# Performance work log

Hardware: AMD Instinct MI355X
Metric: run time of the kernel (lower is better)

Reference implementation:

```python
import jax, jax.numpy as jnp
import numpy as np

B, S, HID = 2, 2048, 4096
NH, NKV, HD = 32, 8, 128
SLIDING_WINDOW = 1024
ROPE_THETA = 10000.0


def setup_inputs() -> dict:
    key = jax.random.key(0)
    ks = jax.random.split(key, 6)
    hidden_states = jax.random.normal(ks[0], (B, S, HID), dtype=jnp.float32)
    attention_mask = jnp.ones((B, S), dtype=jnp.int32)
    position_ids = jnp.broadcast_to(jnp.arange(S, dtype=jnp.int32)[None, :], (B, S))
    sc = 1.0 / np.sqrt(HID)
    q_w = jax.random.normal(ks[1], (HID, NH * HD), dtype=jnp.float32) * sc
    k_w = jax.random.normal(ks[2], (HID, NKV * HD), dtype=jnp.float32) * sc
    v_w = jax.random.normal(ks[3], (HID, NKV * HD), dtype=jnp.float32) * sc
    o_w = jax.random.normal(ks[4], (NH * HD, HID), dtype=jnp.float32) * sc
    return {"hidden_states": hidden_states, "attention_mask": attention_mask,
            "position_ids": position_ids, "q_w": q_w, "k_w": k_w, "v_w": v_w, "o_w": o_w}


def _rotate_half(x):
    return jnp.concatenate((-x[..., x.shape[-1] // 2:], x[..., : x.shape[-1] // 2]), axis=-1)


def _rope_sincos(position_ids):
    # inv_freq over even dims of head_dim; emb = concat(freqs, freqs)
    inv_freq = 1.0 / ROPE_THETA ** (jnp.arange(0, HD, 2, dtype=jnp.float32) / HD)
    freqs = position_ids.astype(jnp.float32)[..., None] * inv_freq  # [B,S,HD/2]
    emb = jnp.concatenate((freqs, freqs), axis=-1)                  # [B,S,HD]
    # broadcast over heads axis: [B,S,1,HD]
    return jnp.sin(emb)[:, :, None, :], jnp.cos(emb)[:, :, None, :]


def reference(hidden_states, attention_mask, position_ids, q_w, k_w, v_w, o_w):
    b, q_len, _ = hidden_states.shape
    n_rep = NH // NKV

    q = (hidden_states @ q_w).reshape(b, q_len, NH, HD)
    k = (hidden_states @ k_w).reshape(b, q_len, NKV, HD)
    v = (hidden_states @ v_w).reshape(b, q_len, NKV, HD)

    sin_pos, cos_pos = _rope_sincos(position_ids)
    q = q * cos_pos + _rotate_half(q) * sin_pos
    k = k * cos_pos + _rotate_half(k) * sin_pos

    # GQA: repeat kv heads (repeat_interleave along head axis)
    k = jnp.repeat(k, n_rep, axis=2)  # [B,S,NH,HD]
    v = jnp.repeat(v, n_rep, axis=2)

    # sliding-window causal mask: j <= i and j >= i - sliding_window
    i = jnp.arange(q_len)[:, None]
    j = jnp.arange(q_len)[None, :]
    band = (j <= i) & (j >= i - SLIDING_WINDOW)           # [Q,K]
    mask = band[None, None] & (attention_mask[:, None, None, :] > 0)  # [B,1,Q,K]

    bias = jnp.where(mask, 0.0, jnp.finfo(jnp.float32).min)

    scale = 1.0 / jnp.sqrt(jnp.asarray(HD, dtype=jnp.float32))
    scores = jnp.einsum('bqhd,bkhd->bhqk', q, k) * scale + bias
    attn_weights = jax.nn.softmax(scores, axis=-1)
    attn_out = jnp.einsum('bhqk,bkhd->bqhd', attn_weights, v)
    attn_out = attn_out.reshape(b, q_len, HID)
    return attn_out @ o_w
```

## Files before the change

kernel.cpp:

```cpp
#include <hip/hip_runtime.h>
#include <stdint.h>
#include <stddef.h>

typedef __bf16 bf16x8 __attribute__((ext_vector_type(8)));
typedef short short8 __attribute__((ext_vector_type(8)));
typedef float floatx4 __attribute__((ext_vector_type(4)));
typedef float f32x16 __attribute__((ext_vector_type(16)));
typedef unsigned short ushort4v __attribute__((ext_vector_type(4)));
typedef unsigned int uint2v __attribute__((ext_vector_type(2)));

__device__ __forceinline__ unsigned short f2bf(float f){
  unsigned int u = __float_as_uint(f);
  u += 0x7fffu + ((u >> 16) & 1u);
  return (unsigned short)(u >> 16);
}
__device__ __forceinline__ float bf2f(unsigned short s){
  return __uint_as_float(((unsigned int)s) << 16);
}
__device__ __forceinline__ void gl2lds16(const void* g, void* l){
  __builtin_amdgcn_global_load_lds((const __attribute__((address_space(1))) void*)g,
                                   (__attribute__((address_space(3))) void*)l, 16, 0, 0);
}

__device__ __forceinline__ void transpose_body(const float* __restrict__ in,
                                               unsigned short* __restrict__ out,
                                               int Kd, int Nd, int bx, int by, int t,
                                               unsigned short* tile){
  int n0 = bx * 64, k0 = by * 64;
#pragma unroll
  for (int it = 0; it < 2; ++it){
    int rr = (t >> 3) + it * 32;
    int cc = t & 7;
    const float* src = in + (size_t)(k0 + rr) * Nd + n0 + cc * 8;
    floatx4 a = *(const floatx4*)src;
    floatx4 b = *(const floatx4*)(src + 4);
    short8 s;
#pragma unroll
    for (int j = 0; j < 4; ++j){ s[j] = (short)f2bf(a[j]); s[j + 4] = (short)f2bf(b[j]); }
    *(short8*)&tile[rr * 80 + cc * 8] = s;
  }
  __syncthreads();
#pragma unroll
  for (int it = 0; it < 2; ++it){
    int nr = (t >> 3) + it * 32;
    int kc = t & 7;
    short8 v;
#pragma unroll
    for (int j = 0; j < 8; ++j) v[j] = (short)tile[(kc * 8 + j) * 80 + nr];
    *(short8*)(out + (size_t)(n0 + nr) * Kd + k0 + kc * 8) = v;
  }
}

__global__ __launch_bounds__(256) void transpose_cvt(const float* __restrict__ in,
                                                     unsigned short* __restrict__ out,
                                                     int Kd, int Nd){
  __shared__ __align__(16) unsigned short tile[64 * 80];
  transpose_body(in, out, Kd, Nd, blockIdx.x, blockIdx.y, threadIdx.x, tile);
}

__global__ __launch_bounds__(256) void prep_fused(const float* __restrict__ hidden,
                                                  unsigned short* __restrict__ hb,
                                                  const float* __restrict__ qw,
                                                  unsigned short* __restrict__ qtw,
                                                  const float* __restrict__ kw,
                                                  unsigned short* __restrict__ kt,
                                                  const float* __restrict__ vw,
                                                  unsigned short* __restrict__ vtw){
  __shared__ __align__(16) unsigned short tile[64 * 80];
  const int bid = blockIdx.x, t = threadIdx.x;
  if (bid < 16384){
    int i = bid * 256 + t;
    floatx4 v = *(const floatx4*)(hidden + (size_t)i * 4);
    ushort4v o;
#pragma unroll
    for (int j = 0; j < 4; ++j) o[j] = f2bf(v[j]);
    *(ushort4v*)(hb + (size_t)i * 4) = o;
  } else if (bid < 20480){
    int b2 = bid - 16384;
    transpose_body(qw, qtw, 4096, 4096, b2 & 63, b2 >> 6, t, tile);
  } else if (bid < 21504){
    int b2 = bid - 20480;
    transpose_body(kw, kt, 4096, 1024, b2 & 15, b2 >> 4, t, tile);
  } else {
    int b2 = bid - 21504;
    transpose_body(vw, vtw, 4096, 1024, b2 & 15, b2 >> 4, t, tile);
  }
}

__global__ __launch_bounds__(256, 2) void gemm_bt128(
    const unsigned short* __restrict__ A,
    const unsigned short* __restrict__ Wq,
    const unsigned short* __restrict__ Wk,
    const unsigned short* __restrict__ Wv,
    unsigned short* __restrict__ oQ,
    unsigned short* __restrict__ oK,
    unsigned short* __restrict__ oVt,
    float* __restrict__ oF, int f32out)
{
  __shared__ __align__(16) unsigned short As[128 * 64];
  __shared__ __align__(16) unsigned short Bs[128 * 64];
  const int tid = threadIdx.x;
  const int w = tid >> 6, lane = tid & 63, quad = lane >> 4, l15 = lane & 15;
  const int wm64 = (w >> 1) * 64, wn64 = (w & 1) * 64;
  const int m0 = blockIdx.y * 128;
  const int n0 = blockIdx.x * 128;

  const unsigned short* Wsrc;
  int nb, region;
  if (n0 < 4096)      { Wsrc = Wq; nb = n0;        region = 0; }
  else if (n0 < 5120) { Wsrc = Wk; nb = n0 - 4096; region = 1; }
  else                { Wsrc = Wv; nb = n0 - 5120; region = 2; }

  floatx4 acc[4][4];
#pragma unroll
  for (int i = 0; i < 4; ++i)
#pragma unroll
    for (int j = 0; j < 4; ++j) acc[i][j] = (floatx4){0.f, 0.f, 0.f, 0.f};

  const int rsub = lane >> 3, csub = lane & 7;

  for (int k0 = 0; k0 < 4096; k0 += 64){
#pragma unroll
    for (int i = 0; i < 4; ++i){
      int u = i * 4 + w;
      int r = u * 8 + rsub;
      gl2lds16(A    + ((size_t)(m0 + r) << 12) + k0 + ((csub ^ (r & 7)) << 3), (char*)As + u * 1024);
      gl2lds16(Wsrc + ((size_t)(nb + r) << 12) + k0 + ((csub ^ (r & 7)) << 3), (char*)Bs + u * 1024);
    }
    __syncthreads();
#pragma unroll
    for (int ks = 0; ks < 2; ++ks){
      bf16x8 af[4], bfr[4];
#pragma unroll
      for (int mt = 0; mt < 4; ++mt){
        int r = wm64 + mt * 16 + l15;
        int kc = ks * 4 + quad;
        af[mt] = *(const bf16x8*)&As[r * 64 + ((kc ^ (r & 7)) << 3)];
      }
#pragma unroll
      for (int nt = 0; nt < 4; ++nt){
        int r = wn64 + nt * 16 + l15;
        int kc = ks * 4 + quad;
        bfr[nt] = *(const bf16x8*)&Bs[r * 64 + ((kc ^ (r & 7)) << 3)];
      }
#pragma unroll
      for (int mt = 0; mt < 4; ++mt)
#pragma unroll
        for (int nt = 0; nt < 4; ++nt)
          acc[mt][nt] = __builtin_amdgcn_mfma_f32_16x16x32_bf16(af[mt], bfr[nt], acc[mt][nt], 0, 0, 0);
    }
    __syncthreads();
  }

  if (region == 0){
    if (f32out){
#pragma unroll
      for (int mt = 0; mt < 4; ++mt)
#pragma unroll
        for (int nt = 0; nt < 4; ++nt){
          int gn = n0 + wn64 + nt * 16 + l15;
#pragma unroll
          for (int rr = 0; rr < 4; ++rr){
            int gm = m0 + wm64 + mt * 16 + quad * 4 + rr;
            oF[((size_t)gm << 12) + gn] = acc[mt][nt][rr];
          }
        }
    } else {
#pragma unroll
      for (int mt = 0; mt < 4; ++mt)
#pragma unroll
        for (int nt = 0; nt < 4; ++nt){
          int gn = n0 + wn64 + nt * 16 + l15;
#pragma unroll
          for (int rr = 0; rr < 4; ++rr){
            int gm = m0 + wm64 + mt * 16 + quad * 4 + rr;
            oQ[((size_t)gm << 12) + gn] = f2bf(acc[mt][nt][rr]);
          }
        }
    }
  } else if (region == 1){
#pragma unroll
    for (int mt = 0; mt < 4; ++mt)
#pragma unroll
      for (int nt = 0; nt < 4; ++nt){
        int gn = n0 - 4096 + wn64 + nt * 16 + l15;
#pragma unroll
        for (int rr = 0; rr < 4; ++rr){
          int gm = m0 + wm64 + mt * 16 + quad * 4 + rr;
          oK[((size_t)gm << 10) + gn] = f2bf(acc[mt][nt][rr]);
        }
      }
  } else {
#pragma unroll
    for (int mt = 0; mt < 4; ++mt){
      int gm0 = m0 + wm64 + mt * 16 + quad * 4;
      int b = gm0 >> 11, s0 = gm0 & 2047;
#pragma unroll
      for (int nt = 0; nt < 4; ++nt){
        int dg = n0 - 5120 + wn64 + nt * 16 + l15;
        int kvh = dg >> 7, d = dg & 127;
        ushort4v pk;
#pragma unroll
        for (int rr = 0; rr < 4; ++rr) pk[rr] = f2bf(acc[mt][nt][rr]);
        *(ushort4v*)(oVt + (((size_t)(b * 8 + kvh) * 128 + d) * 2048 + s0)) = pk;
      }
    }
  }
}

__global__ __launch_bounds__(512, 2) void gemm_bt256(
    const unsigned short* __restrict__ A,
    const unsigned short* __restrict__ Wq,
    const unsigned short* __restrict__ Wk,
    const unsigned short* __restrict__ Wv,
    unsigned short* __restrict__ oQ,
    unsigned short* __restrict__ oK,
    unsigned short* __restrict__ oVt,
    float* __restrict__ oF, int f32out)
{
  __shared__ __align__(16) unsigned short As[2][256 * 64];
  __shared__ __align__(16) unsigned short Bs[2][256 * 64];
  const int tid = threadIdx.x;
  const int w = tid >> 6, lane = tid & 63, quad = lane >> 4, l15 = lane & 15;
  const int wr = w >> 2, wc = w & 3;
  const int m0 = blockIdx.y * 256;
  const int n0 = blockIdx.x * 256;

  const unsigned short* Wsrc;
  int nb, region;
  if (n0 < 4096)      { Wsrc = Wq; nb = n0;        region = 0; }
  else if (n0 < 5120) { Wsrc = Wk; nb = n0 - 4096; region = 1; }
  else                { Wsrc = Wv; nb = n0 - 5120; region = 2; }

  floatx4 acc[8][4];
#pragma unroll
  for (int i = 0; i < 8; ++i)
#pragma unroll
    for (int j = 0; j < 4; ++j) acc[i][j] = (floatx4){0.f, 0.f, 0.f, 0.f};

#define STG(SRC, ROW0, H, DST, K0)                                                     \
  { _Pragma("unroll")                                                                  \
    for (int rep_ = 0; rep_ < 2; ++rep_){                                              \
      int u_ = tid + rep_ * 512;                                                       \
      int r_ = (H) * 128 + (u_ >> 3);                                                  \
      int c_ = u_ & 7;                                                                 \
      gl2lds16((SRC) + ((size_t)((ROW0) + r_) << 12) + (K0) + ((c_ ^ (r_ & 7)) << 3),  \
               (char*)(DST) + (H) * 16384 + (size_t)u_ * 16);                          \
    } }

  STG(A,    m0, 0, &As[0][0], 0);
  STG(Wsrc, nb, 0, &Bs[0][0], 0);
  STG(Wsrc, nb, 1, &Bs[0][0], 0);
  STG(A,    m0, 1, &As[0][0], 0);
  asm volatile("s_waitcnt vmcnt(4)" ::: "memory");
  __builtin_amdgcn_s_barrier();

  for (int t = 0; t < 64; ++t){
    const int cb = t & 1, nbuf = cb ^ 1;
    const int s = (t < 63) ? (t + 1) : 63;
    const int kn = s << 6;
    const unsigned short* Ac = &As[cb][0];
    const unsigned short* Bc = &Bs[cb][0];

    bf16x8 af[4][2], bf0[2][2], bf1[2][2];

#pragma unroll
    for (int i = 0; i < 4; ++i){
      int r = (wr * 4 + i) * 16 + l15;
#pragma unroll
      for (int ks = 0; ks < 2; ++ks){
        int kc = ks * 4 + quad;
        af[i][ks] = *(const bf16x8*)&Ac[r * 64 + ((kc ^ (r & 7)) << 3)];
      }
    }
#pragma unroll
    for (int j = 0; j < 2; ++j){
      int r = (wc * 2 + j) * 16 + l15;
#pragma unroll
      for (int ks = 0; ks < 2; ++ks){
        int kc = ks * 4 + quad;
        bf0[j][ks] = *(const bf16x8*)&Bc[r * 64 + ((kc ^ (r & 7)) << 3)];
      }
    }
    STG(A, m0, 0, &As[nbuf][0], kn);
    __builtin_amdgcn_s_setprio(1);
#pragma unroll
    for (int i = 0; i < 4; ++i)
#pragma unroll
      for (int j = 0; j < 2; ++j)
#pragma unroll
        for (int ks = 0; ks < 2; ++ks)
          acc[i][j] = __builtin_amdgcn_mfma_f32_16x16x32_bf16(af[i][ks], bf0[j][ks], acc[i][j], 0, 0, 0);
    __builtin_amdgcn_s_setprio(0);
    asm volatile("s_waitcnt vmcnt(4)" ::: "memory");
    __builtin_amdgcn_s_barrier();

#pragma unroll
    for (int j = 0; j < 2; ++j){
      int r = (8 + wc * 2 + j) * 16 + l15;
#pragma unroll
      for (int ks = 0; ks < 2; ++ks){
        int kc = ks * 4 + quad;
        bf1[j][ks] = *(const bf16x8*)&Bc[r * 64 + ((kc ^ (r & 7)) << 3)];
      }
    }
    STG(Wsrc, nb, 0, &Bs[nbuf][0], kn);
    __builtin_amdgcn_s_setprio(1);
#pragma unroll
    for (int i = 0; i < 4; ++i)
#pragma unroll
      for (int j = 0; j < 2; ++j)
#pragma unroll
        for (int ks = 0; ks < 2; ++ks)
          acc[i][2 + j] = __builtin_amdgcn_mfma_f32_16x16x32_bf16(af[i][ks], bf1[j][ks], acc[i][2 + j], 0, 0, 0);
    __builtin_amdgcn_s_setprio(0);
    asm volatile("s_waitcnt vmcnt(4)" ::: "memory");
    __builtin_amdgcn_s_barrier();

#pragma unroll
    for (int i = 0; i < 4; ++i){
      int r = (8 + wr * 4 + i) * 16 + l15;
#pragma unroll
      for (int ks = 0; ks < 2; ++ks){
        int kc = ks * 4 + quad;
        af[i][ks] = *(const bf16x8*)&Ac[r * 64 + ((kc ^ (r & 7)) << 3)];
      }
    }
    STG(Wsrc, nb, 1, &Bs[nbuf][0], kn);
    __builtin_amdgcn_s_setprio(1);
#pragma unroll
    for (int i = 0; i < 4; ++i)
#pragma unroll
      for (int j = 0; j < 2; ++j)
#pragma unroll
        for (int ks = 0; ks < 2; ++ks)
          acc[4 + i][2 + j] = __builtin_amdgcn_mfma_f32_16x16x32_bf16(af[i][ks], bf1[j][ks], acc[4 + i][2 + j], 0, 0, 0);
    __builtin_amdgcn_s_setprio(0);
    __builtin_amdgcn_s_barrier();

#pragma unroll
    for (int j = 0; j < 2; ++j){
      int r = (wc * 2 + j) * 16 + l15;
#pragma unroll
      for (int ks = 0; ks < 2; ++ks){
        int kc = ks * 4 + quad;
        bf0[j][ks] = *(const bf16x8*)&Bc[r * 64 + ((kc ^ (r & 7)) << 3)];
      }
    }
    STG(A, m0, 1, &As[nbuf][0], kn);
    __builtin_amdgcn_s_setprio(1);
#pragma unroll
    for (int i = 0; i < 4; ++i)
#pragma unroll
      for (int j = 0; j < 2; ++j)
#pragma unroll
        for (int ks = 0; ks < 2; ++ks)
          acc[4 + i][j] = __builtin_amdgcn_mfma_f32_16x16x32_bf16(af[i][ks], bf0[j][ks], acc[4 + i][j], 0, 0, 0);
    __builtin_amdgcn_s_setprio(0);
    asm volatile("s_waitcnt vmcnt(4)" ::: "memory");
    __builtin_amdgcn_s_barrier();
  }
#undef STG

  if (region == 0){
    if (f32out){
#pragma unroll
      for (int mi = 0; mi < 8; ++mi){
        const int row = (mi >> 2) * 128 + wr * 64 + (mi & 3) * 16 + quad * 4;
#pragma unroll
        for (int nj = 0; nj < 4; ++nj){
          const int gn = n0 + (nj >> 1) * 128 + wc * 32 + (nj & 1) * 16 + l15;
#pragma unroll
          for (int rr = 0; rr < 4; ++rr){
            const int gm = m0 + row + rr;
            oF[((size_t)gm << 12) + gn] = acc[mi][nj][rr];
          }
        }
      }
    } else {
#pragma unroll
      for (int mi = 0; mi < 8; ++mi){
        const int row = (mi >> 2) * 128 + wr * 64 + (mi & 3) * 16 + quad * 4;
#pragma unroll
        for (int nj = 0; nj < 4; ++nj){
          const int gn = n0 + (nj >> 1) * 128 + wc * 32 + (nj & 1) * 16 + l15;
#pragma unroll
          for (int rr = 0; rr < 4; ++rr){
            const int gm = m0 + row + rr;
            oQ[((size_t)gm << 12) + gn] = f2bf(acc[mi][nj][rr]);
          }
        }
      }
    }
  } else if (region == 1){
#pragma unroll
    for (int mi = 0; mi < 8; ++mi){
      const int row = (mi >> 2) * 128 + wr * 64 + (mi & 3) * 16 + quad * 4;
#pragma unroll
      for (int nj = 0; nj < 4; ++nj){
        const int gn = n0 - 4096 + (nj >> 1) * 128 + wc * 32 + (nj & 1) * 16 + l15;
#pragma unroll
        for (int rr = 0; rr < 4; ++rr){
          const int gm = m0 + row + rr;
          oK[((size_t)gm << 10) + gn] = f2bf(acc[mi][nj][rr]);
        }
      }
    }
  } else {
#pragma unroll
    for (int mi = 0; mi < 8; ++mi){
      const int gm0 = m0 + (mi >> 2) * 128 + wr * 64 + (mi & 3) * 16 + quad * 4;
      const int b = gm0 >> 11, s0 = gm0 & 2047;
#pragma unroll
      for (int nj = 0; nj < 4; ++nj){
        const int dg = n0 - 5120 + (nj >> 1) * 128 + wc * 32 + (nj & 1) * 16 + l15;
        const int kvh = dg >> 7, d = dg & 127;
        ushort4v pk;
#pragma unroll
        for (int rr = 0; rr < 4; ++rr) pk[rr] = f2bf(acc[mi][nj][rr]);
        *(ushort4v*)(oVt + (((size_t)(b * 8 + kvh) * 128 + d) * 2048 + s0)) = pk;
      }
    }
  }
}

__global__ void rope_apply_k(unsigned short* __restrict__ Qb, unsigned short* __restrict__ Kb,
                             const int* __restrict__ pos){
  int t = blockIdx.x * 256 + threadIdx.x;
  unsigned short* base;
  int row, ch;
  bool isq = (t < 1048576);
  if (isq){ row = t >> 8; int c = t & 255; base = Qb + ((size_t)row << 12) + (c >> 3) * 128; ch = c & 7; }
  else { int t2 = t - 1048576; row = t2 >> 6; int c = t2 & 63; base = Kb + ((size_t)row << 10) + (c >> 3) * 128; ch = c & 7; }
  float p = (float)pos[row];
  const float qs = 0.08838834764831845f * 1.44269504088896340736f;
  float sc_out = isq ? qs : 1.0f;
  int d0 = ch * 8;
  short8 x0 = *(short8*)(base + d0);
  short8 x1 = *(short8*)(base + d0 + 64);
  short8 y0, y1;
#pragma unroll
  for (int j = 0; j < 8; ++j){
    float ang = p * exp2f(-(float)(d0 + j) * 0.20762050593045952f);
    float sn = sinf(ang), cs = cosf(ang);
    float a  = bf2f((unsigned short)x0[j]);
    float bb = bf2f((unsigned short)x1[j]);
    y0[j] = (short)f2bf((a * cs - bb * sn) * sc_out);
    y1[j] = (short)f2bf((bb * cs + a * sn) * sc_out);
  }
  *(short8*)(base + d0)      = y0;
  *(short8*)(base + d0 + 64) = y1;
}

__global__ __launch_bounds__(256, 2) void flash_swa(
    const unsigned short* __restrict__ Q,
    const unsigned short* __restrict__ K,
    const unsigned short* __restrict__ Vt,
    const int* __restrict__ amask,
    unsigned short* __restrict__ attn)
{
  __shared__ __align__(16) unsigned short Kl[2][64 * 128];
  __shared__ __align__(16) unsigned short Vl[2][128 * 64];
  __shared__ __align__(16) unsigned int   Pl[4][1024];
  const int h = blockIdx.y, b = blockIdx.z;
  const int kv = h >> 2;
  const int tid = threadIdx.x, w = tid >> 6, lane = tid & 63;
  const int l31 = lane & 31, hi = lane >> 5, hi4 = hi << 2;
  const int qb = blockIdx.x * 128;
  const int t0 = qb >> 6;
  const int qw0 = qb + w * 32;
  const int aw = t0 + (w >> 1);

  bool anybad = false;
  {
    const int* ap = amask + b * 2048 + lane * 32;
#pragma unroll
    for (int i = 0; i < 8; ++i){
      int4 mv = *(const int4*)(ap + i * 4);
      anybad |= (mv.x <= 0) | (mv.y <= 0) | (mv.z <= 0) | (mv.w <= 0);
    }
  }
  const bool allv = (__ballot(anybad) == 0ull);

  bf16x8 qf[8];
  {
    const unsigned short* qbase = Q + (((size_t)(b * 2048 + qw0 + l31)) << 12) + h * 128;
#pragma unroll
    for (int ds = 0; ds < 8; ++ds) qf[ds] = *(const bf16x8*)(qbase + ds * 16 + hi * 8);
  }

  f32x16 acco[4];
#pragma unroll
  for (int i = 0; i < 4; ++i)
#pragma unroll
    for (int j = 0; j < 16; ++j) acco[i][j] = 0.f;
  float m_i = -1e30f, l_i = 0.f;

  const int jb0 = (t0 >= 16) ? (t0 - 16) : 0;
  const int jtend = t0 + 1;

#define STAGE_KV(JT, BUF)                                                                  \
  {                                                                                        \
    const int k0s = (JT) * 64;                                                             \
    _Pragma("unroll")                                                                      \
    for (int i_ = 0; i_ < 4; ++i_){                                                        \
      int u_ = i_ * 4 + w;                                                                 \
      int r_ = u_ * 4 + (lane >> 4);                                                       \
      int c_ = lane & 15;                                                                  \
      gl2lds16(K + (((size_t)(b * 2048 + k0s + r_)) << 10) + kv * 128 + ((c_ ^ (r_ & 15)) << 3), \
               (char*)Kl[BUF] + u_ * 1024);                                                \
    }                                                                                      \
    _Pragma("unroll")                                                                      \
    for (int i_ = 0; i_ < 4; ++i_){                                                        \
      int u_ = i_ * 4 + w;                                                                 \
      int d_ = u_ * 8 + (lane >> 3);                                                       \
      int c_ = lane & 7;                                                                   \
      gl2lds16(Vt + ((size_t)(b * 8 + kv) * 128 + d_) * 2048 + k0s + ((c_ ^ (d_ & 7)) << 3), \
               (char*)Vl[BUF] + u_ * 1024);                                                \
    }                                                                                      \
  }

  STAGE_KV(jb0, 0);
  __syncthreads();

  unsigned int* Pw = &Pl[w][0];
  int cur = 0;
  for (int jt = jb0; jt <= jtend; ++jt){
    if (jt < jtend) STAGE_KV(jt + 1, cur ^ 1);

    const bool active = (jt >= aw - 16) && (jt <= aw);
    if (active){
      const int k0 = jt * 64;
      const unsigned short* Klc = Kl[cur];
      const unsigned short* Vlc = Vl[cur];

      f32x16 ps[2];
#pragma unroll
      for (int kb = 0; kb < 2; ++kb)
#pragma unroll
        for (int j = 0; j < 16; ++j) ps[kb][j] = 0.f;

      __builtin_amdgcn_s_setprio(1);
#pragma unroll
      for (int ds = 0; ds < 8; ++ds){
#pragma unroll
        for (int kb = 0; kb < 2; ++kb){
          int r = kb * 32 + l31;
          bf16x8 kf = *(const bf16x8*)&Klc[r * 128 + (((ds * 2 + hi) ^ (r & 15)) << 3)];
          ps[kb] = __builtin_amdgcn_mfma_f32_32x32x16_bf16(kf, qf[ds], ps[kb], 0, 0, 0);
        }
      }
      __builtin_amdgcn_s_setprio(0);

      const bool slow = (jt == aw) || (jt == aw - 16) || (!allv);
      if (slow){
        unsigned long long mb = __ballot(amask[b * 2048 + k0 + lane] > 0);
        int irow = qw0 + l31;
#pragma unroll
        for (int kb = 0; kb < 2; ++kb)
#pragma unroll
          for (int reg = 0; reg < 16; ++reg){
            int jv = k0 + kb * 32 + (reg & 3) + 8 * (reg >> 2) + hi4;
            bool valid = (jv <= irow) && (jv >= irow - 1024) &&
                         (((mb >> (jv & 63)) & 1ull) != 0ull);
            ps[kb][reg] = valid ? ps[kb][reg] : -1e30f;
          }
      }

      float t16[16];
#pragma unroll
      for (int r = 0; r < 16; ++r) t16[r] = fmaxf(ps[0][r], ps[1][r]);
      float t8[8];
#pragma unroll
      for (int r = 0; r < 8; ++r) t8[r] = fmaxf(t16[r], t16[r + 8]);
      float t4[4];
#pragma unroll
      for (int r = 0; r < 4; ++r) t4[r] = fmaxf(t8[r], t8[r + 4]);
      float vm = fmaxf(fmaxf(t4[0], t4[1]), fmaxf(t4[2], t4[3]));
      float vmax = fmaxf(vm, __shfl_xor(vm, 32));

      if (!__all(vmax - m_i <= 8.0f)){
        float mnew = fmaxf(m_i, vmax);
        float alpha = exp2f(m_i - mnew);
        m_i = mnew;
        l_i *= alpha;
#pragma unroll
        for (int db = 0; db < 4; ++db) acco[db] *= alpha;
      }

#pragma unroll
      for (int kb = 0; kb < 2; ++kb)
#pragma unroll
        for (int reg = 0; reg < 16; ++reg) ps[kb][reg] = exp2f(ps[kb][reg] - m_i);

      float s16[16];
#pragma unroll
      for (int r = 0; r < 16; ++r) s16[r] = ps[0][r] + ps[1][r];
      float s8[8];
#pragma unroll
      for (int r = 0; r < 8; ++r) s8[r] = s16[r] + s16[r + 8];
      float s4[4];
#pragma unroll
      for (int r = 0; r < 4; ++r) s4[r] = s8[r] + s8[r + 4];
      float sm = (s4[0] + s4[1]) + (s4[2] + s4[3]);
      l_i += sm + __shfl_xor(sm, 32);

#pragma unroll
      for (int kb = 0; kb < 2; ++kb)
#pragma unroll
        for (int g = 0; g < 4; ++g){
          unsigned p0 = (unsigned)f2bf(ps[kb][g * 4 + 0]) | ((unsigned)f2bf(ps[kb][g * 4 + 1]) << 16);
          unsigned p1 = (unsigned)f2bf(ps[kb][g * 4 + 2]) | ((unsigned)f2bf(ps[kb][g * 4 + 3]) << 16);
          int ch = (kb * 4 + g) ^ (l31 & 7);
          uint2v pv_; pv_[0] = p0; pv_[1] = p1;
          *(uint2v*)&Pw[l31 * 32 + ch * 4 + hi * 2] = pv_;
        }
      bf16x8 pa[4];
#pragma unroll
      for (int ks = 0; ks < 4; ++ks)
        pa[ks] = *(const bf16x8*)&Pw[l31 * 32 + (((ks * 2 + hi) ^ (l31 & 7)) << 2)];

      __builtin_amdgcn_s_setprio(1);
#pragma unroll
      for (int ks = 0; ks < 4; ++ks){
#pragma unroll
        for (int db = 0; db < 4; ++db){
          int d = db * 32 + l31;
          bf16x8 vf = *(const bf16x8*)&Vlc[d * 64 + (((ks * 2 + hi) ^ (d & 7)) << 3)];
          acco[db] = __builtin_amdgcn_mfma_f32_32x32x16_bf16(vf, pa[ks], acco[db], 0, 0, 0);
        }
      }
      __builtin_amdgcn_s_setprio(0);
    }

    __syncthreads();
    cur ^= 1;
  }
#undef STAGE_KV

  float invl = 1.f / l_i;
  unsigned short* Ep = ((unsigned short*)Kl) + w * 4096;
  {
    const int q = l31;
#pragma unroll
    for (int db = 0; db < 4; ++db)
#pragma unroll
      for (int reg = 0; reg < 16; ++reg){
        int dc = db * 4 + (reg >> 2);
        int dl = (reg & 3) + hi4;
        Ep[q * 128 + ((dc ^ (q & 15)) << 3) + dl] = f2bf(acco[db][reg] * invl);
      }
  }
  {
    const int rr_ = lane >> 4, cc = lane & 15;
#pragma unroll
    for (int p8 = 0; p8 < 8; ++p8){
      int q = p8 * 4 + rr_;
      short8 vv = *(const short8*)&Ep[q * 128 + ((cc ^ (q & 15)) << 3)];
      size_t off = (((size_t)(b * 2048 + qb + w * 32 + q)) << 12) + h * 128 + cc * 8;
      *(short8*)(attn + off) = vv;
    }
  }
}

extern "C" void kernel_launch(void* const* d_in, const int* in_sizes, int n_in,
                              void* d_out, int out_size, void* d_ws, size_t ws_size,
                              hipStream_t stream){
  const float* hidden = (const float*)d_in[0];
  const int* amask = (const int*)d_in[1];
  const int* pos   = (const int*)d_in[2];
  const float* qw = (const float*)d_in[3];
  const float* kw = (const float*)d_in[4];
  const float* vw = (const float*)d_in[5];
  const float* ow = (const float*)d_in[6];

  char* ws = (char*)d_ws;
  unsigned short* hb   = (unsigned short*)(ws + 0);
  unsigned short* qt   = (unsigned short*)(ws + 33554432);
  unsigned short* kt   = (unsigned short*)(ws + 67108864);
  unsigned short* vtw  = (unsigned short*)(ws + 75497472);
  unsigned short* Qb   = (unsigned short*)(ws + 83886080);
  unsigned short* Kb   = (unsigned short*)(ws + 117440512);
  unsigned short* Vtb  = (unsigned short*)(ws + 125829120);
  unsigned short* ot   = hb;
  unsigned short* attn = qt;
  float* outp = (float*)d_out;

  hipLaunchKernelGGL(prep_fused, dim3(22528), dim3(256), 0, stream,
                     hidden, hb, qw, qt, kw, kt, vw, vtw);
  hipLaunchKernelGGL(gemm_bt128, dim3(48, 32), dim3(256), 0, stream,
                     hb, qt, kt, vtw, Qb, Kb, Vtb, (float*)nullptr, 0);
  hipLaunchKernelGGL(transpose_cvt, dim3(64, 64), dim3(256), 0, stream, ow, ot, 4096, 4096);
  hipLaunchKernelGGL(rope_apply_k, dim3(5120), dim3(256), 0, stream, Qb, Kb, pos);
  hipLaunchKernelGGL(flash_swa, dim3(16, 32, 2), dim3(256), 0, stream, Qb, Kb, Vtb, amask, attn);
  hipLaunchKernelGGL(gemm_bt256, dim3(16, 16), dim3(512), 0, stream,
                     attn, ot, ot, ot, nullptr, nullptr, nullptr, outp, 1);
}
```

Measured before the change: 707.7 us.

## Split fused prep kernel into separate launches and swizzle QKV GEMM block order

Replaces the single fused preprocessing kernel with four separate launches: one f32-to-bf16 convert and three transpose-convert passes. Remaps the QKV projection GEMM's linear block index through an 8-way swizzle so that consecutively scheduled blocks share A and B tiles in cache. The swizzle targets L2/MALL reuse in the largest GEMM. The split adds launch overhead and removes the branch-divergent fused grid, so its intent is less clear.

```diff
diff --git a/kernel.cpp b/kernel.cpp
--- a/kernel.cpp
+++ b/kernel.cpp
@@ -22,11 +22,22 @@
                                    (__attribute__((address_space(3))) void*)l, 16, 0, 0);
 }
 
-__device__ __forceinline__ void transpose_body(const float* __restrict__ in,
-                                               unsigned short* __restrict__ out,
-                                               int Kd, int Nd, int bx, int by, int t,
-                                               unsigned short* tile){
-  int n0 = bx * 64, k0 = by * 64;
+__global__ __launch_bounds__(256) void conv_f32_bf16(const float* __restrict__ in,
+                                                     unsigned short* __restrict__ out){
+  int t = blockIdx.x * 256 + threadIdx.x;
+  floatx4 v = *(const floatx4*)(in + (size_t)t * 4);
+  ushort4v o;
+#pragma unroll
+  for (int j = 0; j < 4; ++j) o[j] = f2bf(v[j]);
+  *(ushort4v*)(out + (size_t)t * 4) = o;
+}
+
+__global__ __launch_bounds__(256) void transpose_cvt(const float* __restrict__ in,
+                                                     unsigned short* __restrict__ out,
+                                                     int Kd, int Nd){
+  __shared__ __align__(16) unsigned short tile[64 * 80];
+  int n0 = blockIdx.x * 64, k0 = blockIdx.y * 64;
+  int t = threadIdx.x;
 #pragma unroll
   for (int it = 0; it < 2; ++it){
     int rr = (t >> 3) + it * 32;
@@ -48,42 +59,6 @@
 #pragma unroll
     for (int j = 0; j < 8; ++j) v[j] = (short)tile[(kc * 8 + j) * 80 + nr];
     *(short8*)(out + (size_t)(n0 + nr) * Kd + k0 + kc * 8) = v;
-  }
-}
-
-__global__ __launch_bounds__(256) void transpose_cvt(const float* __restrict__ in,
-                                                     unsigned short* __restrict__ out,
-                                                     int Kd, int Nd){
-  __shared__ __align__(16) unsigned short tile[64 * 80];
-  transpose_body(in, out, Kd, Nd, blockIdx.x, blockIdx.y, threadIdx.x, tile);
-}
-
-__global__ __launch_bounds__(256) void prep_fused(const float* __restrict__ hidden,
-                                                  unsigned short* __restrict__ hb,
-                                                  const float* __restrict__ qw,
-                                                  unsigned short* __restrict__ qtw,
-                                                  const float* __restrict__ kw,
-                                                  unsigned short* __restrict__ kt,
-                                                  const float* __restrict__ vw,
-                                                  unsigned short* __restrict__ vtw){
-  __shared__ __align__(16) unsigned short tile[64 * 80];
-  const int bid = blockIdx.x, t = threadIdx.x;
-  if (bid < 16384){
-    int i = bid * 256 + t;
-    floatx4 v = *(const floatx4*)(hidden + (size_t)i * 4);
-    ushort4v o;
-#pragma unroll
-    for (int j = 0; j < 4; ++j) o[j] = f2bf(v[j]);
-    *(ushort4v*)(hb + (size_t)i * 4) = o;
-  } else if (bid < 20480){
-    int b2 = bid - 16384;
-    transpose_body(qw, qtw, 4096, 4096, b2 & 63, b2 >> 6, t, tile);
-  } else if (bid < 21504){
-    int b2 = bid - 20480;
-    transpose_body(kw, kt, 4096, 1024, b2 & 15, b2 >> 4, t, tile);
-  } else {
-    int b2 = bid - 21504;
-    transpose_body(vw, vtw, 4096, 1024, b2 & 15, b2 >> 4, t, tile);
   }
 }
 
@@ -102,8 +77,10 @@
   const int tid = threadIdx.x;
   const int w = tid >> 6, lane = tid & 63, quad = lane >> 4, l15 = lane & 15;
   const int wm64 = (w >> 1) * 64, wn64 = (w & 1) * 64;
-  const int m0 = blockIdx.y * 128;
-  const int n0 = blockIdx.x * 128;
+  const int lin = blockIdx.y * 48 + blockIdx.x;
+  const int swz = (lin & 7) * 192 + (lin >> 3);
+  const int m0 = (swz / 48) * 128;
+  const int n0 = (swz % 48) * 128;
 
   const unsigned short* Wsrc;
   int nb, region;
@@ -686,8 +663,10 @@
   unsigned short* attn = qt;
   float* outp = (float*)d_out;
 
-  hipLaunchKernelGGL(prep_fused, dim3(22528), dim3(256), 0, stream,
-                     hidden, hb, qw, qt, kw, kt, vw, vtw);
+  hipLaunchKernelGGL(conv_f32_bf16, dim3(16384), dim3(256), 0, stream, hidden, hb);
+  hipLaunchKernelGGL(transpose_cvt, dim3(64, 64), dim3(256), 0, stream, qw, qt, 4096, 4096);
+  hipLaunchKernelGGL(transpose_cvt, dim3(16, 64), dim3(256), 0, stream, kw, kt, 4096, 1024);
+  hipLaunchKernelGGL(transpose_cvt, dim3(16, 64), dim3(256), 0, stream, vw, vtw, 4096, 1024);
   hipLaunchKernelGGL(gemm_bt128, dim3(48, 32), dim3(256), 0, stream,
                      hb, qt, kt, vtw, Qb, Kb, Vtb, (float*)nullptr, 0);
   hipLaunchKernelGGL(transpose_cvt, dim3(64, 64), dim3(256), 0, stream, ow, ot, 4096, 4096);
```

Result: slower. 754.4 us (+6.6%).
